# Performance work log

Measured on AMD Instinct MI355X. Metric: run time of the kernel, lower is better.

Reference implementation:

```python
import jax, jax.numpy as jnp
import numpy as np

HID = 64
PRE = 14


def _lstm_last(x, Wih, Whh, b):
    # x: (B, T, F) batch_first; single-layer torch LSTM; returns last hidden (B, H)
    H = Whh.shape[1]
    def step(carry, xt):
        h, c = carry
        g = xt @ Wih.T + h @ Whh.T + b  # gates order i,f,g,o (torch convention)
        i, f, gg, o = jnp.split(g, 4, axis=-1)
        c = jax.nn.sigmoid(f) * c + jax.nn.sigmoid(i) * jnp.tanh(gg)
        h = jax.nn.sigmoid(o) * jnp.tanh(c)
        return (h, c), None
    h0 = jnp.zeros((x.shape[0], H), x.dtype)
    (h, _), _ = jax.lax.scan(step, (h0, h0), jnp.swapaxes(x, 0, 1))
    return h


def _sircell(beta, gamma, c, sir):
    # beta,gamma: (B,N,1); c: (B,N,N); sir: (B,N,3); beta_incorporated=False branch
    eps = 1e-8
    S, I, R = sir[..., 0:1], sir[..., 1:2], sir[..., 2:3]
    Ntot = jnp.maximum(S + I + R, eps)
    infection = c @ I                      # (B,N,1) graph diffusion of infected
    dS = -beta * S / Ntot * infection
    dI = -dS - gamma * I
    dR = gamma * I
    S_t = jnp.maximum(S + dS, 0.0)
    I_t = jnp.maximum(I + dI, 0.0)
    R_t = jnp.maximum(R + dR, 0.0)
    scale = Ntot / jnp.maximum(S_t + I_t + R_t, eps)
    I_new = jnp.maximum(-dS, 0.0)
    return jnp.concatenate([I_new, S_t * scale, I_t * scale, R_t * scale], axis=-1)


def reference(x_s, x, bWih, bWhh, bb, bfW, bfb, gWih, gWhh, gb, gfW, gfb, cWih, cWhh, cb, cfW, cfb):
    B, T, N, F = x_s.shape
    P = bfW.shape[0]
    xs = jnp.transpose(x_s, (0, 2, 1, 3)).reshape(B * N, T, F)
    betas = jax.nn.sigmoid(_lstm_last(xs, bWih, bWhh, bb) @ bfW.T + bfb).reshape(B, N, P, 1)
    gammas = jax.nn.sigmoid(_lstm_last(xs, gWih, gWhh, gb) @ gfW.T + gfb).reshape(B, N, P, 1)
    xst = jnp.transpose(x_s, (0, 2, 1, 3))                       # (B,N,T,F)
    Hi = jnp.broadcast_to(xst[:, :, None], (B, N, N, T, F))
    Hj = jnp.broadcast_to(xst[:, None], (B, N, N, T, F))
    edge = jnp.concatenate([Hi, Hj], -1).reshape(B * N * N, T, 2 * F)
    cij = jax.nn.sigmoid(_lstm_last(edge, cWih, cWhh, cb) @ cfW.T + cfb).reshape(B, N, N, P)
    cij = jax.nn.softmax(jnp.transpose(cij, (0, 3, 1, 2)), axis=-1)  # (B,P,N,N)
    cs = jnp.transpose(cij, (0, 2, 1, 3))                            # (B,N,P,N)

    def step(sir, inp):
        bt, gt, ct = inp
        nsir = _sircell(bt, gt, ct, sir)
        return nsir[:, :, 1:], nsir

    _, outs = jax.lax.scan(
        step, x[:, -1],
        (jnp.transpose(betas, (2, 0, 1, 3)),
         jnp.transpose(gammas, (2, 0, 1, 3)),
         jnp.transpose(cs, (2, 0, 1, 3))))
    out = jnp.transpose(outs, (1, 0, 2, 3))                          # (B,P,N,4)
    epi = jnp.transpose(jnp.concatenate([betas, gammas, cs], -1), (0, 2, 1, 3))  # (B,P,N,N+2)
    return out[..., 2:3], epi, out[..., 1:], out[..., 0:1]


def setup_inputs() -> dict:
    key = jax.random.key(0)
    ks = jax.random.split(key, 20)
    B, T, N, F = 4, 12, 128, 3
    H, P = HID, PRE
    s = 1.0 / np.sqrt(H)
    def u(k, shape):
        return jax.random.uniform(k, shape, jnp.float32, -s, s)
    inp = {
        'x_s': jax.random.normal(ks[0], (B, T, N, F), jnp.float32),
        'x': jax.random.uniform(ks[1], (B, T, N, F), jnp.float32),
        'bWih': u(ks[2], (4 * H, F)), 'bWhh': u(ks[3], (4 * H, H)), 'bb': u(ks[4], (4 * H,)),
        'bfW': u(ks[5], (P, H)), 'bfb': u(ks[6], (P,)),
        'gWih': u(ks[7], (4 * H, F)), 'gWhh': u(ks[8], (4 * H, H)), 'gb': u(ks[9], (4 * H,)),
        'gfW': u(ks[10], (P, H)), 'gfb': u(ks[11], (P,)),
        'cWih': u(ks[12], (4 * H, 2 * F)), 'cWhh': u(ks[13], (4 * H, H)), 'cb': u(ks[14], (4 * H,)),
        'cfW': u(ks[15], (P, H)), 'cfb': u(ks[16], (P,)),
    }
    return inp
```

## Files before the change

### kernel.cpp

```cpp
#include <hip/hip_runtime.h>

#define TT 12
#define NN 128
#define BB 4
#define PP 14

typedef __attribute__((ext_vector_type(8))) short short8;
typedef __attribute__((ext_vector_type(4))) float f32x4;
typedef __attribute__((ext_vector_type(2))) float float2v;
typedef __attribute__((ext_vector_type(2))) unsigned uint2v;

__device__ inline unsigned short f2bf(float x){
  unsigned u = __builtin_bit_cast(unsigned, x);
  u += 0x7fffu + ((u >> 16) & 1u);
  return (unsigned short)(u >> 16);
}
__device__ inline float bf2f(unsigned short h){
  unsigned u = ((unsigned)h) << 16;
  return __builtin_bit_cast(float, u);
}
__device__ inline float fexp2(float x){ return __builtin_amdgcn_exp2f(x); }
__device__ inline float frcp(float x){ return __builtin_amdgcn_rcpf(x); }
__device__ inline float sigf(float x){ return frcp(1.0f + fexp2(x * -1.44269504f)); }

__device__ inline float2v exp2v(float2v x){
  float2v r; r[0]=__builtin_amdgcn_exp2f(x[0]); r[1]=__builtin_amdgcn_exp2f(x[1]); return r;
}
__device__ inline float2v rcpv(float2v x){
  float2v r; r[0]=__builtin_amdgcn_rcpf(x[0]); r[1]=__builtin_amdgcn_rcpf(x[1]); return r;
}

__global__ __launch_bounds__(256) void lstm_all(
    const float* __restrict__ x_s,
    const float* __restrict__ bWih, const float* __restrict__ bWhh, const float* __restrict__ bb_,
    const float* __restrict__ bfW,  const float* __restrict__ bfb,
    const float* __restrict__ gWih, const float* __restrict__ gWhh, const float* __restrict__ gb_,
    const float* __restrict__ gfW,  const float* __restrict__ gfb,
    const float* __restrict__ cWih, const float* __restrict__ cWhh, const float* __restrict__ cb_,
    const float* __restrict__ cfW,  const float* __restrict__ cfb,
    float* __restrict__ out_epi)
{
  __shared__ __align__(16) char hbuf[2*4096];
  __shared__ __align__(16) unsigned short xext[TT*32*8];
  __shared__ float fw_lds[PP*64];
  __shared__ float fb_lds[PP];

  const int tid = threadIdx.x;
  const int l = tid & 63, w = tid >> 6;
  const int col = l & 15, q = l >> 4;

  const int rot = (col & 7) << 4;
  const int r0offA = col*128 + ((  0 + (q<<4) + rot) & 127);
  const int r1offA = col*128 + (( 64 + (q<<4) + rot) & 127);
  const int wroffA = col*128 + ((w*32 + q*8 + rot) & 127);
  const int r0offB = r0offA + 2048;
  const int r1offB = r1offA + 2048;
  const int wroffB = wroffA + 2048;

  int g0 = blockIdx.x << 1;
  int mode; const float *Wih, *Whh, *bias, *fW, *fb;
  if (g0 < 4096)      { mode=0; Wih=cWih; Whh=cWhh; bias=cb_; fW=cfW; fb=cfb; }
  else if (g0 < 4128) { mode=1; g0-=4096; Wih=bWih; Whh=bWhh; bias=bb_; fW=bfW; fb=bfb; }
  else                { mode=2; g0-=4128; Wih=gWih; Whh=gWhh; bias=gb_; fW=gfW; fb=gfb; }

  int b, i=0, s0;
  if (mode==0) { b = g0 >> 10; int rem = g0 & 1023; i = rem >> 3; s0 = (rem & 7) << 4; }
  else         { b = g0 >> 3; s0 = (g0 & 7) << 4; }

  for (int task = tid; task < TT*32; task += 256) {
    int t = task >> 5, m = task & 31;
    unsigned short* dst = &xext[(t*32+m)*8];
    float v0=0,v1=0,v2=0,v3=0,v4=0,v5=0,v6=0,v7=0;
    if (mode==0) {
      const float* xi = x_s + ((b*TT + t)*NN + i)*3;
      const float* xj = x_s + ((b*TT + t)*NN + (s0+m))*3;
      v0=xi[0]; v1=xi[1]; v2=xi[2]; v3=xj[0]; v4=xj[1]; v5=xj[2]; v6=1.f;
    } else {
      const float* xn = x_s + ((b*TT + t)*NN + (s0+m))*3;
      v0=xn[0]; v1=xn[1]; v2=xn[2]; v3=1.f;
    }
    dst[0]=f2bf(v0); dst[1]=f2bf(v1); dst[2]=f2bf(v2); dst[3]=f2bf(v3);
    dst[4]=f2bf(v4); dst[5]=f2bf(v5); dst[6]=f2bf(v6); dst[7]=f2bf(v7);
  }
  for (int idx = tid; idx < 1024; idx += 256) ((unsigned*)hbuf)[idx] = 0;
  for (int idx = tid; idx < PP*64; idx += 256) fw_lds[idx] = fW[idx];
  if (tid < PP) fb_lds[tid] = fb[tid];

  short8 Aw[4][2]; short8 Ax[4];
  #pragma unroll
  for (int gt = 0; gt < 4; ++gt) {
    float sc = (gt==2) ? 2.88539008f : -1.44269504f;
    int gate = gt*64 + w*16 + col;
    #pragma unroll
    for (int kt = 0; kt < 2; ++kt) {
      const float* src = Whh + gate*64 + kt*32 + q*8;
      short8 fr;
      #pragma unroll
      for (int jj = 0; jj < 8; ++jj) fr[jj] = (short)f2bf(src[jj]*sc);
      Aw[gt][kt] = fr;
    }
    short8 ax = {0,0,0,0,0,0,0,0};
    if (q == 0) {
      if (mode==0) {
        ax[0]=(short)f2bf(Wih[gate*6+0]*sc); ax[1]=(short)f2bf(Wih[gate*6+1]*sc); ax[2]=(short)f2bf(Wih[gate*6+2]*sc);
        ax[3]=(short)f2bf(Wih[gate*6+3]*sc); ax[4]=(short)f2bf(Wih[gate*6+4]*sc); ax[5]=(short)f2bf(Wih[gate*6+5]*sc);
        ax[6]=(short)f2bf(bias[gate]*sc);
      } else {
        ax[0]=(short)f2bf(Wih[gate*3+0]*sc); ax[1]=(short)f2bf(Wih[gate*3+1]*sc); ax[2]=(short)f2bf(Wih[gate*3+2]*sc);
        ax[3]=(short)f2bf(bias[gate]*sc);
      }
    }
    Ax[gt] = ax;
  }

  __syncthreads();

  float2v cA0 = {0.f,0.f}, cA1 = {0.f,0.f}, cB0 = {0.f,0.f}, cB1 = {0.f,0.f};

#define MM(acc, aop, bop) acc = __builtin_amdgcn_mfma_f32_16x16x32_bf16(aop, bop, acc, 0,0,0)
#define CELL(cvar, hvar, fF, fI, fG, fO) { \
    float2v Ei = exp2v(fI), Ef = exp2v(fF), Eg = exp2v(fG), Eo = exp2v(fO); \
    float2v t1 = (Ei + 1.0f) * (Eg + 1.0f); \
    float2v pf = Ef + 1.0f; \
    float2v num = cvar * t1 + pf * (Eg - 1.0f); \
    cvar = num * rcpv(pf * t1); \
    float2v Ec = exp2v(cvar * 2.88539008f); \
    hvar = (Ec - 1.0f) * rcpv((Ec + 1.0f) * (Eo + 1.0f)); }

  for (int t = 0; t < TT; ++t) {
    const char* rb = hbuf + ((t & 1) ? 4096 : 0);
    char* wbp      = hbuf + ((t & 1) ? 0 : 4096);
    short8 b0a = *(const short8*)(rb + r0offA);
    short8 b1a = *(const short8*)(rb + r1offA);
    short8 b0b = *(const short8*)(rb + r0offB);
    short8 b1b = *(const short8*)(rb + r1offB);
    short8 bxa = *(const short8*)&xext[(t*32 + col)*8];
    short8 bxb = *(const short8*)&xext[(t*32 + 16 + col)*8];
    f32x4 Fa = {0.f,0.f,0.f,0.f}, Ia = Fa, Ga = Fa, Oa = Fa;
    f32x4 Fb = Fa, Ib = Fa, Gb = Fa, Ob = Fa;
    MM(Fa, Aw[1][0], b0a); MM(Fb, Aw[1][0], b0b);
    MM(Ia, Aw[0][0], b0a); MM(Ib, Aw[0][0], b0b);
    MM(Ga, Aw[2][0], b0a); MM(Gb, Aw[2][0], b0b);
    MM(Oa, Aw[3][0], b0a); MM(Ob, Aw[3][0], b0b);
    MM(Fa, Aw[1][1], b1a); MM(Fb, Aw[1][1], b1b);
    MM(Ia, Aw[0][1], b1a); MM(Ib, Aw[0][1], b1b);
    MM(Ga, Aw[2][1], b1a); MM(Gb, Aw[2][1], b1b);
    MM(Oa, Aw[3][1], b1a); MM(Ob, Aw[3][1], b1b);
    MM(Fa, Ax[1], bxa);    MM(Fb, Ax[1], bxb);
    MM(Ia, Ax[0], bxa);    MM(Ib, Ax[0], bxb);
    MM(Ga, Ax[2], bxa);    MM(Gb, Ax[2], bxb);
    MM(Oa, Ax[3], bxa);    MM(Ob, Ax[3], bxb);

    {
      float2v f0 = {Fa[0],Fa[1]}, f1 = {Fa[2],Fa[3]};
      float2v i0 = {Ia[0],Ia[1]}, i1 = {Ia[2],Ia[3]};
      float2v g0v = {Ga[0],Ga[1]}, g1v = {Ga[2],Ga[3]};
      float2v o0 = {Oa[0],Oa[1]}, o1 = {Oa[2],Oa[3]};
      float2v h0, h1;
      CELL(cA0, h0, f0, i0, g0v, o0);
      CELL(cA1, h1, f1, i1, g1v, o1);
      unsigned plo, phi;
      asm("v_cvt_pk_bf16_f32 %0, %1, %2" : "=v"(plo) : "v"(h0[0]), "v"(h0[1]));
      asm("v_cvt_pk_bf16_f32 %0, %1, %2" : "=v"(phi) : "v"(h1[0]), "v"(h1[1]));
      uint2v pv = {plo, phi};
      *(uint2v*)(wbp + wroffA) = pv;
    }
    {
      float2v f0 = {Fb[0],Fb[1]}, f1 = {Fb[2],Fb[3]};
      float2v i0 = {Ib[0],Ib[1]}, i1 = {Ib[2],Ib[3]};
      float2v g0v = {Gb[0],Gb[1]}, g1v = {Gb[2],Gb[3]};
      float2v o0 = {Ob[0],Ob[1]}, o1 = {Ob[2],Ob[3]};
      float2v h0, h1;
      CELL(cB0, h0, f0, i0, g0v, o0);
      CELL(cB1, h1, f1, i1, g1v, o1);
      unsigned plo, phi;
      asm("v_cvt_pk_bf16_f32 %0, %1, %2" : "=v"(plo) : "v"(h0[0]), "v"(h0[1]));
      asm("v_cvt_pk_bf16_f32 %0, %1, %2" : "=v"(phi) : "v"(h1[0]), "v"(h1[1]));
      uint2v pv = {plo, phi};
      *(uint2v*)(wbp + wroffB) = pv;
    }
    __syncthreads();
  }
#undef MM
#undef CELL

  const char* hfin = hbuf;
  for (int task = tid; task < 32*PP; task += 256) {
    int seq = task & 31, p = task >> 5;
    int rot2 = (seq & 7) << 4;
    float dot = fb_lds[p];
    #pragma unroll
    for (int kc = 0; kc < 8; ++kc) {
      short8 v = *(const short8*)(hfin + seq*128 + (((kc<<4) + rot2) & 127));
      #pragma unroll
      for (int jj = 0; jj < 8; ++jj)
        dot += bf2f((unsigned short)v[jj]) * fw_lds[p*64 + kc*8 + jj];
    }
    float val = sigf(dot);
    if (mode==0) {
      out_epi[(size_t)((b*PP + p)*NN + i)*130 + 2 + (s0+seq)] = val;
    } else if (mode==1) {
      out_epi[(size_t)((b*PP + p)*NN + (s0+seq))*130 + 0] = val;
    } else {
      out_epi[(size_t)((b*PP + p)*NN + (s0+seq))*130 + 1] = val;
    }
  }
}

__global__ __launch_bounds__(256) void softmax_epi(float* __restrict__ out_epi)
{
  int row = blockIdx.x*4 + (threadIdx.x >> 6);
  int l = threadIdx.x & 63;
  float* epi = out_epi + (size_t)row*130;
  float v0 = epi[2+l], v1 = epi[2+64+l];
  float e0 = fexp2(v0*1.44269504f), e1 = fexp2(v1*1.44269504f);
  float s = e0 + e1;
  #pragma unroll
  for (int off = 32; off; off >>= 1) s += __shfl_xor(s, off);
  float inv = frcp(s);
  epi[2+l] = e0*inv; epi[2+64+l] = e1*inv;
}

__global__ __launch_bounds__(1024) void sir_scan(
    const float* __restrict__ x,
    const float* __restrict__ epi,
    float* __restrict__ out0, float* __restrict__ out2, float* __restrict__ out3)
{
  __shared__ float Ish[NN];
  int b = blockIdx.x;
  int tid = threadIdx.x;
  int i = tid >> 3, q = tid & 7;
  const float* x0 = x + ((b*TT + 11)*NN + i)*3;
  float S = x0[0], I = x0[1], R = x0[2];
  if (q == 0) Ish[i] = I;

  float2v v[8], vn[8];
  {
    const float* crow = epi + (size_t)((b*PP + 0)*NN + i)*130 + 2 + q*16;
    #pragma unroll
    for (int jj = 0; jj < 8; ++jj) v[jj] = *(const float2v*)(crow + jj*2);
  }
  __syncthreads();
  for (int p = 0; p < PP; ++p) {
    if (p+1 < PP) {
      const float* crow = epi + (size_t)((b*PP + p+1)*NN + i)*130 + 2 + q*16;
      #pragma unroll
      for (int jj = 0; jj < 8; ++jj) vn[jj] = *(const float2v*)(crow + jj*2);
    }
    float part = 0.f;
    #pragma unroll
    for (int jj = 0; jj < 8; ++jj)
      part += v[jj][0]*Ish[q*16 + jj*2] + v[jj][1]*Ish[q*16 + jj*2 + 1];
    part += __shfl_xor(part, 1);
    part += __shfl_xor(part, 2);
    part += __shfl_xor(part, 4);
    __syncthreads();
    if (q == 0) {
      const float* erow = epi + (size_t)((b*PP + p)*NN + i)*130;
      float beta  = erow[0];
      float gamma = erow[1];
      float Ntot = fmaxf(S+I+R, 1e-8f);
      float dS = -beta*S/Ntot*part;
      float dI = -dS - gamma*I;
      float dR = gamma*I;
      float St = fmaxf(S+dS, 0.f), It = fmaxf(I+dI, 0.f), Rt = fmaxf(R+dR, 0.f);
      float scale = Ntot / fmaxf(St+It+Rt, 1e-8f);
      float Inew = fmaxf(-dS, 0.f);
      int o = (b*PP+p)*NN + i;
      float Sn = St*scale, In = It*scale, Rn = Rt*scale;
      out0[o] = In;
      out2[o*3+0] = Sn; out2[o*3+1] = In; out2[o*3+2] = Rn;
      out3[o] = Inew;
      S = Sn; I = In; R = Rn;
      Ish[i] = I;
    }
    #pragma unroll
    for (int jj = 0; jj < 8; ++jj) v[jj] = vn[jj];
    __syncthreads();
  }
}

extern "C" void kernel_launch(void* const* d_in, const int* in_sizes, int n_in,
                              void* d_out, int out_size, void* d_ws, size_t ws_size,
                              hipStream_t stream) {
  const float* x_s  = (const float*)d_in[0];
  const float* x    = (const float*)d_in[1];
  const float* bWih = (const float*)d_in[2];
  const float* bWhh = (const float*)d_in[3];
  const float* bb_  = (const float*)d_in[4];
  const float* bfW  = (const float*)d_in[5];
  const float* bfb  = (const float*)d_in[6];
  const float* gWih = (const float*)d_in[7];
  const float* gWhh = (const float*)d_in[8];
  const float* gb_  = (const float*)d_in[9];
  const float* gfW  = (const float*)d_in[10];
  const float* gfb  = (const float*)d_in[11];
  const float* cWih = (const float*)d_in[12];
  const float* cWhh = (const float*)d_in[13];
  const float* cb_  = (const float*)d_in[14];
  const float* cfW  = (const float*)d_in[15];
  const float* cfb  = (const float*)d_in[16];

  float* out  = (float*)d_out;
  float* out0 = out;
  float* epi  = out + 7168;
  float* out2 = out + 7168 + 931840;
  float* out3 = out + 7168 + 931840 + 21504;

  hipLaunchKernelGGL(lstm_all, dim3(2080), dim3(256), 0, stream,
      x_s, bWih,bWhh,bb_,bfW,bfb, gWih,gWhh,gb_,gfW,gfb, cWih,cWhh,cb_,cfW,cfb,
      epi);
  hipLaunchKernelGGL(softmax_epi, dim3(1792), dim3(256), 0, stream, epi);
  hipLaunchKernelGGL(sir_scan, dim3(4), dim3(1024), 0, stream,
      x, epi, out0, out2, out3);
}
```

Baseline: 110.2 us.

## Double LSTM block size and stage gate weights in LDS instead of registers

The LSTM kernel now processes 64 sequences per 512-thread block instead of 32 per 256-thread block. Recurrent and input weight fragments are staged once in shared memory and reread each timestep, rather than kept in registers. This cuts per-block weight setup and register pressure, at the cost of extra LDS traffic inside the time loop and half as many blocks. It also merges pairs of reciprocals into one rcp plus two multiplies, and stores the final projection weights as bf16 in LDS, which slightly changes numerics.

```diff
diff --git a/kernel.cpp b/kernel.cpp
--- a/kernel.cpp
+++ b/kernel.cpp
@@ -26,11 +26,12 @@
 __device__ inline float2v exp2v(float2v x){
   float2v r; r[0]=__builtin_amdgcn_exp2f(x[0]); r[1]=__builtin_amdgcn_exp2f(x[1]); return r;
 }
-__device__ inline float2v rcpv(float2v x){
-  float2v r; r[0]=__builtin_amdgcn_rcpf(x[0]); r[1]=__builtin_amdgcn_rcpf(x[1]); return r;
-}
-
-__global__ __launch_bounds__(256) void lstm_all(
+__device__ inline float2v rcpv1(float2v x){
+  float r = frcp(x[0]*x[1]);
+  float2v o; o[0] = x[1]*r; o[1] = x[0]*r; return o;
+}
+
+__global__ __launch_bounds__(512) void lstm_all(
     const float* __restrict__ x_s,
     const float* __restrict__ bWih, const float* __restrict__ bWhh, const float* __restrict__ bb_,
     const float* __restrict__ bfW,  const float* __restrict__ bfb,
@@ -40,36 +41,41 @@
     const float* __restrict__ cfW,  const float* __restrict__ cfb,
     float* __restrict__ out_epi)
 {
-  __shared__ __align__(16) char hbuf[2*4096];
-  __shared__ __align__(16) unsigned short xext[TT*32*8];
-  __shared__ float fw_lds[PP*64];
+  __shared__ __align__(16) unsigned short wfrag[48*64*8];
+  __shared__ __align__(16) char hbuf[2*8192];
+  __shared__ __align__(16) unsigned short xext[TT*64*8];
+  __shared__ unsigned short fw_lds[PP*64];
   __shared__ float fb_lds[PP];
 
   const int tid = threadIdx.x;
-  const int l = tid & 63, w = tid >> 6;
+  const int l = tid & 63;
+  const int wv = tid >> 6;
+  const int w_h = wv & 3;
+  const int half = wv >> 2;
   const int col = l & 15, q = l >> 4;
 
   const int rot = (col & 7) << 4;
-  const int r0offA = col*128 + ((  0 + (q<<4) + rot) & 127);
-  const int r1offA = col*128 + (( 64 + (q<<4) + rot) & 127);
-  const int wroffA = col*128 + ((w*32 + q*8 + rot) & 127);
-  const int r0offB = r0offA + 2048;
-  const int r1offB = r1offA + 2048;
-  const int wroffB = wroffA + 2048;
-
-  int g0 = blockIdx.x << 1;
+  const int rowA = half*32 + col,  rowB = half*32 + 16 + col;
+  const int r0offA = rowA*128 + (((q<<4) + rot) & 127);
+  const int r1offA = rowA*128 + ((64 + (q<<4) + rot) & 127);
+  const int r0offB = rowB*128 + (((q<<4) + rot) & 127);
+  const int r1offB = rowB*128 + ((64 + (q<<4) + rot) & 127);
+  const int wroffA = rowA*128 + ((w_h*32 + q*8 + rot) & 127);
+  const int wroffB = rowB*128 + ((w_h*32 + q*8 + rot) & 127);
+
+  int g = blockIdx.x;
   int mode; const float *Wih, *Whh, *bias, *fW, *fb;
-  if (g0 < 4096)      { mode=0; Wih=cWih; Whh=cWhh; bias=cb_; fW=cfW; fb=cfb; }
-  else if (g0 < 4128) { mode=1; g0-=4096; Wih=bWih; Whh=bWhh; bias=bb_; fW=bfW; fb=bfb; }
-  else                { mode=2; g0-=4128; Wih=gWih; Whh=gWhh; bias=gb_; fW=gfW; fb=gfb; }
+  if (g < 1024)      { mode=0; Wih=cWih; Whh=cWhh; bias=cb_; fW=cfW; fb=cfb; }
+  else if (g < 1032) { mode=1; g-=1024; Wih=bWih; Whh=bWhh; bias=bb_; fW=bfW; fb=bfb; }
+  else               { mode=2; g-=1032; Wih=gWih; Whh=gWhh; bias=gb_; fW=gfW; fb=gfb; }
 
   int b, i=0, s0;
-  if (mode==0) { b = g0 >> 10; int rem = g0 & 1023; i = rem >> 3; s0 = (rem & 7) << 4; }
-  else         { b = g0 >> 3; s0 = (g0 & 7) << 4; }
-
-  for (int task = tid; task < TT*32; task += 256) {
-    int t = task >> 5, m = task & 31;
-    unsigned short* dst = &xext[(t*32+m)*8];
+  if (mode==0) { b = g >> 8; int rem = g & 255; i = rem >> 1; s0 = (rem & 1) << 6; }
+  else         { b = g >> 1; s0 = (g & 1) << 6; }
+
+  for (int task = tid; task < TT*64; task += 512) {
+    int t = task >> 6, m = task & 63;
+    unsigned short* dst = &xext[(t*64+m)*8];
     float v0=0,v1=0,v2=0,v3=0,v4=0,v5=0,v6=0,v7=0;
     if (mode==0) {
       const float* xi = x_s + ((b*TT + t)*NN + i)*3;
@@ -82,35 +88,32 @@
     dst[0]=f2bf(v0); dst[1]=f2bf(v1); dst[2]=f2bf(v2); dst[3]=f2bf(v3);
     dst[4]=f2bf(v4); dst[5]=f2bf(v5); dst[6]=f2bf(v6); dst[7]=f2bf(v7);
   }
-  for (int idx = tid; idx < 1024; idx += 256) ((unsigned*)hbuf)[idx] = 0;
-  for (int idx = tid; idx < PP*64; idx += 256) fw_lds[idx] = fW[idx];
+  for (int idx = tid; idx < 2048; idx += 512) ((unsigned*)hbuf)[idx] = 0;
+  for (int idx = tid; idx < PP*64; idx += 512) fw_lds[idx] = f2bf(fW[idx]);
   if (tid < PP) fb_lds[tid] = fb[tid];
 
-  short8 Aw[4][2]; short8 Ax[4];
-  #pragma unroll
-  for (int gt = 0; gt < 4; ++gt) {
+  for (int slot = tid; slot < 48*64; slot += 512) {
+    int tile = slot >> 6, lane = slot & 63;
+    int w_hs = tile / 12, rem = tile % 12, gt = rem / 3, kt = rem % 3;
     float sc = (gt==2) ? 2.88539008f : -1.44269504f;
-    int gate = gt*64 + w*16 + col;
-    #pragma unroll
-    for (int kt = 0; kt < 2; ++kt) {
-      const float* src = Whh + gate*64 + kt*32 + q*8;
-      short8 fr;
+    int gate = gt*64 + w_hs*16 + (lane & 15);
+    int qq = lane >> 4;
+    short8 fr = {0,0,0,0,0,0,0,0};
+    if (kt < 2) {
+      const float* src = Whh + gate*64 + kt*32 + qq*8;
       #pragma unroll
       for (int jj = 0; jj < 8; ++jj) fr[jj] = (short)f2bf(src[jj]*sc);
-      Aw[gt][kt] = fr;
-    }
-    short8 ax = {0,0,0,0,0,0,0,0};
-    if (q == 0) {
+    } else if (qq == 0) {
       if (mode==0) {
-        ax[0]=(short)f2bf(Wih[gate*6+0]*sc); ax[1]=(short)f2bf(Wih[gate*6+1]*sc); ax[2]=(short)f2bf(Wih[gate*6+2]*sc);
-        ax[3]=(short)f2bf(Wih[gate*6+3]*sc); ax[4]=(short)f2bf(Wih[gate*6+4]*sc); ax[5]=(short)f2bf(Wih[gate*6+5]*sc);
-        ax[6]=(short)f2bf(bias[gate]*sc);
+        fr[0]=(short)f2bf(Wih[gate*6+0]*sc); fr[1]=(short)f2bf(Wih[gate*6+1]*sc); fr[2]=(short)f2bf(Wih[gate*6+2]*sc);
+        fr[3]=(short)f2bf(Wih[gate*6+3]*sc); fr[4]=(short)f2bf(Wih[gate*6+4]*sc); fr[5]=(short)f2bf(Wih[gate*6+5]*sc);
+        fr[6]=(short)f2bf(bias[gate]*sc);
       } else {
-        ax[0]=(short)f2bf(Wih[gate*3+0]*sc); ax[1]=(short)f2bf(Wih[gate*3+1]*sc); ax[2]=(short)f2bf(Wih[gate*3+2]*sc);
-        ax[3]=(short)f2bf(bias[gate]*sc);
+        fr[0]=(short)f2bf(Wih[gate*3+0]*sc); fr[1]=(short)f2bf(Wih[gate*3+1]*sc); fr[2]=(short)f2bf(Wih[gate*3+2]*sc);
+        fr[3]=(short)f2bf(bias[gate]*sc);
       }
     }
-    Ax[gt] = ax;
+    *(short8*)&wfrag[slot*8] = fr;
   }
 
   __syncthreads();
@@ -123,33 +126,32 @@
     float2v t1 = (Ei + 1.0f) * (Eg + 1.0f); \
     float2v pf = Ef + 1.0f; \
     float2v num = cvar * t1 + pf * (Eg - 1.0f); \
-    cvar = num * rcpv(pf * t1); \
+    cvar = num * rcpv1(pf * t1); \
     float2v Ec = exp2v(cvar * 2.88539008f); \
-    hvar = (Ec - 1.0f) * rcpv((Ec + 1.0f) * (Eo + 1.0f)); }
+    hvar = (Ec - 1.0f) * rcpv1((Ec + 1.0f) * (Eo + 1.0f)); }
+#define GATETILE(gt, accA, accB) { \
+    short8 f0 = *(const short8*)&wfrag[((w_h*12 + (gt)*3 + 0)*64 + l)*8]; \
+    short8 f1 = *(const short8*)&wfrag[((w_h*12 + (gt)*3 + 1)*64 + l)*8]; \
+    short8 fx = *(const short8*)&wfrag[((w_h*12 + (gt)*3 + 2)*64 + l)*8]; \
+    MM(accA, f0, b0a); MM(accB, f0, b0b); \
+    MM(accA, f1, b1a); MM(accB, f1, b1b); \
+    MM(accA, fx, bxa); MM(accB, fx, bxb); }
 
   for (int t = 0; t < TT; ++t) {
-    const char* rb = hbuf + ((t & 1) ? 4096 : 0);
-    char* wbp      = hbuf + ((t & 1) ? 0 : 4096);
+    const char* rb = hbuf + ((t & 1) ? 8192 : 0);
+    char* wbp      = hbuf + ((t & 1) ? 0 : 8192);
     short8 b0a = *(const short8*)(rb + r0offA);
     short8 b1a = *(const short8*)(rb + r1offA);
     short8 b0b = *(const short8*)(rb + r0offB);
     short8 b1b = *(const short8*)(rb + r1offB);
-    short8 bxa = *(const short8*)&xext[(t*32 + col)*8];
-    short8 bxb = *(const short8*)&xext[(t*32 + 16 + col)*8];
+    short8 bxa = *(const short8*)&xext[(t*64 + half*32 + col)*8];
+    short8 bxb = *(const short8*)&xext[(t*64 + half*32 + 16 + col)*8];
     f32x4 Fa = {0.f,0.f,0.f,0.f}, Ia = Fa, Ga = Fa, Oa = Fa;
     f32x4 Fb = Fa, Ib = Fa, Gb = Fa, Ob = Fa;
-    MM(Fa, Aw[1][0], b0a); MM(Fb, Aw[1][0], b0b);
-    MM(Ia, Aw[0][0], b0a); MM(Ib, Aw[0][0], b0b);
-    MM(Ga, Aw[2][0], b0a); MM(Gb, Aw[2][0], b0b);
-    MM(Oa, Aw[3][0], b0a); MM(Ob, Aw[3][0], b0b);
-    MM(Fa, Aw[1][1], b1a); MM(Fb, Aw[1][1], b1b);
-    MM(Ia, Aw[0][1], b1a); MM(Ib, Aw[0][1], b1b);
-    MM(Ga, Aw[2][1], b1a); MM(Gb, Aw[2][1], b1b);
-    MM(Oa, Aw[3][1], b1a); MM(Ob, Aw[3][1], b1b);
-    MM(Fa, Ax[1], bxa);    MM(Fb, Ax[1], bxb);
-    MM(Ia, Ax[0], bxa);    MM(Ib, Ax[0], bxb);
-    MM(Ga, Ax[2], bxa);    MM(Gb, Ax[2], bxb);
-    MM(Oa, Ax[3], bxa);    MM(Ob, Ax[3], bxb);
+    GATETILE(1, Fa, Fb);
+    GATETILE(0, Ia, Ib);
+    GATETILE(2, Ga, Gb);
+    GATETILE(3, Oa, Ob);
 
     {
       float2v f0 = {Fa[0],Fa[1]}, f1 = {Fa[2],Fa[3]};
@@ -183,10 +185,11 @@
   }
 #undef MM
 #undef CELL
+#undef GATETILE
 
   const char* hfin = hbuf;
-  for (int task = tid; task < 32*PP; task += 256) {
-    int seq = task & 31, p = task >> 5;
+  for (int task = tid; task < 64*PP; task += 512) {
+    int seq = task & 63, p = task >> 6;
     int rot2 = (seq & 7) << 4;
     float dot = fb_lds[p];
     #pragma unroll
@@ -194,7 +197,7 @@
       short8 v = *(const short8*)(hfin + seq*128 + (((kc<<4) + rot2) & 127));
       #pragma unroll
       for (int jj = 0; jj < 8; ++jj)
-        dot += bf2f((unsigned short)v[jj]) * fw_lds[p*64 + kc*8 + jj];
+        dot += bf2f((unsigned short)v[jj]) * bf2f(fw_lds[p*64 + kc*8 + jj]);
     }
     float val = sigf(dot);
     if (mode==0) {
@@ -307,7 +310,7 @@
   float* out2 = out + 7168 + 931840;
   float* out3 = out + 7168 + 931840 + 21504;
 
-  hipLaunchKernelGGL(lstm_all, dim3(2080), dim3(256), 0, stream,
+  hipLaunchKernelGGL(lstm_all, dim3(1040), dim3(512), 0, stream,
       x_s, bWih,bWhh,bb_,bfW,bfb, gWih,gWhh,gb_,gfW,gfb, cWih,cWhh,cb_,cfW,cfb,
       epi);
   hipLaunchKernelGGL(softmax_epi, dim3(1792), dim3(256), 0, stream, epi);
```

After: 107.4 us. -2.5%, faster.
